# Kernel tuning notes

Hardware: AMD Instinct MI355X
Metric: run time of the kernel (lower is better)

The kernel has to match this reference:

```python
import jax, jax.numpy as jnp
import numpy as np

B, T, D = 32, 2048, 512

def setup_inputs() -> dict:
    key = jax.random.key(0)
    k1, k2, k3 = jax.random.split(key, 3)
    return {
        "query": jax.random.normal(k1, (B, D), dtype=jnp.float32),
        "key": jax.random.normal(k2, (B, T, D), dtype=jnp.float32),
        "value": jax.random.normal(k3, (B, T, D), dtype=jnp.float32),
    }

def reference(query, key, value):
    # energy: [B, T] = bmm(key [B,T,D], query [B,D,1]).squeeze
    energy = jnp.einsum("btd,bd->bt", key, query)
    attention = jax.nn.softmax(energy, axis=1)  # over T, no scaling/masking (faithful)
    # context: [B, D] = bmm(attention [B,1,T], value [B,T,D]).squeeze
    out = jnp.einsum("bt,btd->bd", attention, value)
    return (out, attention)
```

## Files before the change

kernel.cpp:

```cpp
#include <hip/hip_runtime.h>

#define B_ 32
#define T_ 2048
#define D_ 512

__global__ __launch_bounds__(256) void energy_kernel(
    const float* __restrict__ q,
    const float* __restrict__ key,
    float* __restrict__ energy)
{
    const int b    = blockIdx.x >> 6;
    const int t0   = (blockIdx.x & 63) * 32;
    const int wave = threadIdx.x >> 6;
    const int lane = threadIdx.x & 63;

    const float4 qv0 = ((const float4*)q)[b * 128 + lane];
    const float4 qv1 = ((const float4*)q)[b * 128 + 64 + lane];

    const int trow = t0 + wave * 8;
    const float4* kbase = (const float4*)key + ((size_t)b * T_ + trow) * 128;

#pragma unroll 4
    for (int r = 0; r < 8; ++r) {
        const float4 k0 = kbase[r * 128 + lane];
        const float4 k1 = kbase[r * 128 + 64 + lane];
        float acc = k0.x * qv0.x + k0.y * qv0.y + k0.z * qv0.z + k0.w * qv0.w
                  + k1.x * qv1.x + k1.y * qv1.y + k1.z * qv1.z + k1.w * qv1.w;
#pragma unroll
        for (int off = 32; off >= 1; off >>= 1)
            acc += __shfl_down(acc, off);
        if (lane == 0)
            energy[b * T_ + trow + r] = acc;
    }
}

__global__ __launch_bounds__(256) void softmax_kernel(
    const float* __restrict__ energy,
    float* __restrict__ attn)
{
    const int b = blockIdx.x;
    const int wave = threadIdx.x >> 6;
    const int lane = threadIdx.x & 63;

    const float4* e4 = (const float4*)(energy + b * T_);
    float4 v0 = e4[threadIdx.x * 2 + 0];
    float4 v1 = e4[threadIdx.x * 2 + 1];

    float m = fmaxf(fmaxf(fmaxf(v0.x, v0.y), fmaxf(v0.z, v0.w)),
                    fmaxf(fmaxf(v1.x, v1.y), fmaxf(v1.z, v1.w)));
#pragma unroll
    for (int off = 32; off >= 1; off >>= 1)
        m = fmaxf(m, __shfl_xor(m, off));
    __shared__ float redm[4];
    if (lane == 0) redm[wave] = m;
    __syncthreads();
    m = fmaxf(fmaxf(redm[0], redm[1]), fmaxf(redm[2], redm[3]));

    float4 x0, x1;
    x0.x = __expf(v0.x - m); x0.y = __expf(v0.y - m);
    x0.z = __expf(v0.z - m); x0.w = __expf(v0.w - m);
    x1.x = __expf(v1.x - m); x1.y = __expf(v1.y - m);
    x1.z = __expf(v1.z - m); x1.w = __expf(v1.w - m);
    float s = x0.x + x0.y + x0.z + x0.w + x1.x + x1.y + x1.z + x1.w;
#pragma unroll
    for (int off = 32; off >= 1; off >>= 1)
        s += __shfl_xor(s, off);
    __shared__ float reds[4];
    if (lane == 0) reds[wave] = s;
    __syncthreads();
    s = reds[0] + reds[1] + reds[2] + reds[3];

    const float inv = 1.f / s;
    x0.x *= inv; x0.y *= inv; x0.z *= inv; x0.w *= inv;
    x1.x *= inv; x1.y *= inv; x1.z *= inv; x1.w *= inv;

    float4* a4 = (float4*)(attn + b * T_);
    a4[threadIdx.x * 2 + 0] = x0;
    a4[threadIdx.x * 2 + 1] = x1;
}

__global__ __launch_bounds__(256) void context_partial_kernel(
    const float* __restrict__ attn,
    const float* __restrict__ value,
    float* __restrict__ partial)
{
    __shared__ float  attn_s[64];
    __shared__ float4 red4[128];

    const int b     = blockIdx.x >> 5;
    const int chunk = blockIdx.x & 31;
    const int t0    = chunk * 64;

    if (threadIdx.x < 64)
        attn_s[threadIdx.x] = attn[b * T_ + t0 + threadIdx.x];
    __syncthreads();

    const int tg = threadIdx.x >> 7;
    const int d4 = threadIdx.x & 127;

    const float4* v4 = (const float4*)value + ((size_t)b * T_ + t0 + tg) * 128 + d4;
    float4 acc = {0.f, 0.f, 0.f, 0.f};
#pragma unroll 8
    for (int i = 0; i < 32; ++i) {
        const float a = attn_s[2 * i + tg];
        const float4 vv = v4[i * 256];
        acc.x += a * vv.x; acc.y += a * vv.y;
        acc.z += a * vv.z; acc.w += a * vv.w;
    }

    if (tg == 1) red4[d4] = acc;
    __syncthreads();
    if (tg == 0) {
        const float4 o = red4[d4];
        acc.x += o.x; acc.y += o.y; acc.z += o.z; acc.w += o.w;
        ((float4*)partial)[((size_t)b * 32 + chunk) * 128 + d4] = acc;
    }
}

__global__ __launch_bounds__(128) void reduce_kernel(
    const float* __restrict__ partial,
    float* __restrict__ out)
{
    const int b  = blockIdx.x;
    const int d4 = threadIdx.x;
    float4 s = {0.f, 0.f, 0.f, 0.f};
#pragma unroll
    for (int c = 0; c < 32; ++c) {
        const float4 p = ((const float4*)partial)[((size_t)b * 32 + c) * 128 + d4];
        s.x += p.x; s.y += p.y; s.z += p.z; s.w += p.w;
    }
    ((float4*)out)[b * 128 + d4] = s;
}

extern "C" void kernel_launch(void* const* d_in, const int* in_sizes, int n_in,
                              void* d_out, int out_size, void* d_ws, size_t ws_size,
                              hipStream_t stream)
{
    const float* q     = (const float*)d_in[0];
    const float* key   = (const float*)d_in[1];
    const float* value = (const float*)d_in[2];

    float* out  = (float*)d_out;
    float* attn = out + B_ * D_;

    float* energy  = (float*)d_ws;
    float* partial = energy + B_ * T_;

    energy_kernel<<<B_ * 64, 256, 0, stream>>>(q, key, energy);
    softmax_kernel<<<B_, 256, 0, stream>>>(energy, attn);
    context_partial_kernel<<<B_ * 32, 256, 0, stream>>>(attn, value, partial);
    reduce_kernel<<<B_, 128, 0, stream>>>(partial, out);
}
```

Before: 288.0 us.

## Fuse four attention kernels into one cooperative kernel with grid syncs

Replaces the energy, softmax, context-partial and reduce kernels with a single cooperative kernel of 1024 blocks separated by grid-wide syncs. The aim is to remove the launch overhead and inter-kernel gaps of four launches. The costs are three grid.sync barriers, and the softmax and reduce phases run on only 32 blocks while the rest sit idle. The energy phase now does 16 rows per wave instead of 8, with half as many blocks.

```diff
diff --git a/kernel.cpp b/kernel.cpp
--- a/kernel.cpp
+++ b/kernel.cpp
@@ -1,135 +1,135 @@
 #include <hip/hip_runtime.h>
+#include <hip/hip_cooperative_groups.h>
+
+namespace cg = cooperative_groups;
 
 #define B_ 32
 #define T_ 2048
 #define D_ 512
+#define GRID_ 1024
 
-__global__ __launch_bounds__(256) void energy_kernel(
+__global__ __launch_bounds__(256, 4) void fused_attention_kernel(
     const float* __restrict__ q,
     const float* __restrict__ key,
-    float* __restrict__ energy)
-{
-    const int b    = blockIdx.x >> 6;
-    const int t0   = (blockIdx.x & 63) * 32;
-    const int wave = threadIdx.x >> 6;
-    const int lane = threadIdx.x & 63;
-
-    const float4 qv0 = ((const float4*)q)[b * 128 + lane];
-    const float4 qv1 = ((const float4*)q)[b * 128 + 64 + lane];
-
-    const int trow = t0 + wave * 8;
-    const float4* kbase = (const float4*)key + ((size_t)b * T_ + trow) * 128;
-
-#pragma unroll 4
-    for (int r = 0; r < 8; ++r) {
-        const float4 k0 = kbase[r * 128 + lane];
-        const float4 k1 = kbase[r * 128 + 64 + lane];
-        float acc = k0.x * qv0.x + k0.y * qv0.y + k0.z * qv0.z + k0.w * qv0.w
-                  + k1.x * qv1.x + k1.y * qv1.y + k1.z * qv1.z + k1.w * qv1.w;
-#pragma unroll
-        for (int off = 32; off >= 1; off >>= 1)
-            acc += __shfl_down(acc, off);
-        if (lane == 0)
-            energy[b * T_ + trow + r] = acc;
-    }
-}
-
-__global__ __launch_bounds__(256) void softmax_kernel(
-    const float* __restrict__ energy,
-    float* __restrict__ attn)
-{
-    const int b = blockIdx.x;
-    const int wave = threadIdx.x >> 6;
-    const int lane = threadIdx.x & 63;
-
-    const float4* e4 = (const float4*)(energy + b * T_);
-    float4 v0 = e4[threadIdx.x * 2 + 0];
-    float4 v1 = e4[threadIdx.x * 2 + 1];
-
-    float m = fmaxf(fmaxf(fmaxf(v0.x, v0.y), fmaxf(v0.z, v0.w)),
-                    fmaxf(fmaxf(v1.x, v1.y), fmaxf(v1.z, v1.w)));
-#pragma unroll
-    for (int off = 32; off >= 1; off >>= 1)
-        m = fmaxf(m, __shfl_xor(m, off));
-    __shared__ float redm[4];
-    if (lane == 0) redm[wave] = m;
-    __syncthreads();
-    m = fmaxf(fmaxf(redm[0], redm[1]), fmaxf(redm[2], redm[3]));
-
-    float4 x0, x1;
-    x0.x = __expf(v0.x - m); x0.y = __expf(v0.y - m);
-    x0.z = __expf(v0.z - m); x0.w = __expf(v0.w - m);
-    x1.x = __expf(v1.x - m); x1.y = __expf(v1.y - m);
-    x1.z = __expf(v1.z - m); x1.w = __expf(v1.w - m);
-    float s = x0.x + x0.y + x0.z + x0.w + x1.x + x1.y + x1.z + x1.w;
-#pragma unroll
-    for (int off = 32; off >= 1; off >>= 1)
-        s += __shfl_xor(s, off);
-    __shared__ float reds[4];
-    if (lane == 0) reds[wave] = s;
-    __syncthreads();
-    s = reds[0] + reds[1] + reds[2] + reds[3];
-
-    const float inv = 1.f / s;
-    x0.x *= inv; x0.y *= inv; x0.z *= inv; x0.w *= inv;
-    x1.x *= inv; x1.y *= inv; x1.z *= inv; x1.w *= inv;
-
-    float4* a4 = (float4*)(attn + b * T_);
-    a4[threadIdx.x * 2 + 0] = x0;
-    a4[threadIdx.x * 2 + 1] = x1;
-}
-
-__global__ __launch_bounds__(256) void context_partial_kernel(
-    const float* __restrict__ attn,
     const float* __restrict__ value,
+    float* __restrict__ out,
+    float* __restrict__ attn,
+    float* __restrict__ energy,
     float* __restrict__ partial)
 {
+    cg::grid_group grid = cg::this_grid();
+
+    __shared__ float  redm[4];
+    __shared__ float  reds[4];
     __shared__ float  attn_s[64];
     __shared__ float4 red4[128];
 
-    const int b     = blockIdx.x >> 5;
-    const int chunk = blockIdx.x & 31;
-    const int t0    = chunk * 64;
+    const int b_blk = blockIdx.x >> 5;
+    const int sub   = blockIdx.x & 31;
+    const int wave  = threadIdx.x >> 6;
+    const int lane  = threadIdx.x & 63;
 
-    if (threadIdx.x < 64)
-        attn_s[threadIdx.x] = attn[b * T_ + t0 + threadIdx.x];
-    __syncthreads();
-
-    const int tg = threadIdx.x >> 7;
-    const int d4 = threadIdx.x & 127;
-
-    const float4* v4 = (const float4*)value + ((size_t)b * T_ + t0 + tg) * 128 + d4;
-    float4 acc = {0.f, 0.f, 0.f, 0.f};
-#pragma unroll 8
-    for (int i = 0; i < 32; ++i) {
-        const float a = attn_s[2 * i + tg];
-        const float4 vv = v4[i * 256];
-        acc.x += a * vv.x; acc.y += a * vv.y;
-        acc.z += a * vv.z; acc.w += a * vv.w;
+    {
+        const float4 qv0 = ((const float4*)q)[b_blk * 128 + lane];
+        const float4 qv1 = ((const float4*)q)[b_blk * 128 + 64 + lane];
+        const int t0 = sub * 64 + wave * 16;
+        const float4* kbase = (const float4*)key + ((size_t)b_blk * T_ + t0) * 128;
+#pragma unroll 4
+        for (int r = 0; r < 16; ++r) {
+            const float4 k0 = kbase[r * 128 + lane];
+            const float4 k1 = kbase[r * 128 + 64 + lane];
+            float acc = k0.x * qv0.x + k0.y * qv0.y + k0.z * qv0.z + k0.w * qv0.w
+                      + k1.x * qv1.x + k1.y * qv1.y + k1.z * qv1.z + k1.w * qv1.w;
+#pragma unroll
+            for (int off = 32; off >= 1; off >>= 1)
+                acc += __shfl_down(acc, off);
+            if (lane == 0)
+                energy[b_blk * T_ + t0 + r] = acc;
+        }
     }
 
-    if (tg == 1) red4[d4] = acc;
-    __syncthreads();
-    if (tg == 0) {
-        const float4 o = red4[d4];
-        acc.x += o.x; acc.y += o.y; acc.z += o.z; acc.w += o.w;
-        ((float4*)partial)[((size_t)b * 32 + chunk) * 128 + d4] = acc;
+    grid.sync();
+
+    if (blockIdx.x < B_) {
+        const int b = blockIdx.x;
+        const float4* e4 = (const float4*)(energy + b * T_);
+        float4 v0 = e4[threadIdx.x * 2 + 0];
+        float4 v1 = e4[threadIdx.x * 2 + 1];
+
+        float m = fmaxf(fmaxf(fmaxf(v0.x, v0.y), fmaxf(v0.z, v0.w)),
+                        fmaxf(fmaxf(v1.x, v1.y), fmaxf(v1.z, v1.w)));
+#pragma unroll
+        for (int off = 32; off >= 1; off >>= 1)
+            m = fmaxf(m, __shfl_xor(m, off));
+        if (lane == 0) redm[wave] = m;
+        __syncthreads();
+        m = fmaxf(fmaxf(redm[0], redm[1]), fmaxf(redm[2], redm[3]));
+
+        float4 x0, x1;
+        x0.x = __expf(v0.x - m); x0.y = __expf(v0.y - m);
+        x0.z = __expf(v0.z - m); x0.w = __expf(v0.w - m);
+        x1.x = __expf(v1.x - m); x1.y = __expf(v1.y - m);
+        x1.z = __expf(v1.z - m); x1.w = __expf(v1.w - m);
+        float s = x0.x + x0.y + x0.z + x0.w + x1.x + x1.y + x1.z + x1.w;
+#pragma unroll
+        for (int off = 32; off >= 1; off >>= 1)
+            s += __shfl_xor(s, off);
+        if (lane == 0) reds[wave] = s;
+        __syncthreads();
+        s = reds[0] + reds[1] + reds[2] + reds[3];
+
+        const float inv = 1.f / s;
+        x0.x *= inv; x0.y *= inv; x0.z *= inv; x0.w *= inv;
+        x1.x *= inv; x1.y *= inv; x1.z *= inv; x1.w *= inv;
+
+        float4* a4 = (float4*)(attn + b * T_);
+        a4[threadIdx.x * 2 + 0] = x0;
+        a4[threadIdx.x * 2 + 1] = x1;
     }
-}
 
-__global__ __launch_bounds__(128) void reduce_kernel(
-    const float* __restrict__ partial,
-    float* __restrict__ out)
-{
-    const int b  = blockIdx.x;
-    const int d4 = threadIdx.x;
-    float4 s = {0.f, 0.f, 0.f, 0.f};
+    grid.sync();
+
+    {
+        const int t0 = sub * 64;
+        if (threadIdx.x < 64)
+            attn_s[threadIdx.x] = attn[b_blk * T_ + t0 + threadIdx.x];
+        __syncthreads();
+
+        const int tg = threadIdx.x >> 7;
+        const int d4 = threadIdx.x & 127;
+
+        const float4* v4 = (const float4*)value + ((size_t)b_blk * T_ + t0 + tg) * 128 + d4;
+        float4 acc = {0.f, 0.f, 0.f, 0.f};
+#pragma unroll 8
+        for (int i = 0; i < 32; ++i) {
+            const float a = attn_s[2 * i + tg];
+            const float4 vv = v4[i * 256];
+            acc.x += a * vv.x; acc.y += a * vv.y;
+            acc.z += a * vv.z; acc.w += a * vv.w;
+        }
+
+        if (tg == 1) red4[d4] = acc;
+        __syncthreads();
+        if (tg == 0) {
+            const float4 o = red4[d4];
+            acc.x += o.x; acc.y += o.y; acc.z += o.z; acc.w += o.w;
+            ((float4*)partial)[((size_t)b_blk * 32 + sub) * 128 + d4] = acc;
+        }
+    }
+
+    grid.sync();
+
+    if (blockIdx.x < B_ && threadIdx.x < 128) {
+        const int b  = blockIdx.x;
+        const int d4 = threadIdx.x;
+        float4 s = {0.f, 0.f, 0.f, 0.f};
 #pragma unroll
-    for (int c = 0; c < 32; ++c) {
-        const float4 p = ((const float4*)partial)[((size_t)b * 32 + c) * 128 + d4];
-        s.x += p.x; s.y += p.y; s.z += p.z; s.w += p.w;
+        for (int c = 0; c < 32; ++c) {
+            const float4 p = ((const float4*)partial)[((size_t)b * 32 + c) * 128 + d4];
+            s.x += p.x; s.y += p.y; s.z += p.z; s.w += p.w;
+        }
+        ((float4*)out)[b * 128 + d4] = s;
     }
-    ((float4*)out)[b * 128 + d4] = s;
 }
 
 extern "C" void kernel_launch(void* const* d_in, const int* in_sizes, int n_in,
@@ -146,8 +146,10 @@
     float* energy  = (float*)d_ws;
     float* partial = energy + B_ * T_;
 
-    energy_kernel<<<B_ * 64, 256, 0, stream>>>(q, key, energy);
-    softmax_kernel<<<B_, 256, 0, stream>>>(energy, attn);
-    context_partial_kernel<<<B_ * 32, 256, 0, stream>>>(attn, value, partial);
-    reduce_kernel<<<B_, 128, 0, stream>>>(partial, out);
+    void* args[] = {
+        (void*)&q, (void*)&key, (void*)&value,
+        (void*)&out, (void*)&attn, (void*)&energy, (void*)&partial
+    };
+    hipLaunchCooperativeKernel((void*)fused_attention_kernel,
+                               dim3(GRID_), dim3(256), args, 0, stream);
 }
```

After: 601.7 us. 109% more time.

## Fuse softmax into energy and context kernels using per-chunk online stats and atomics

Applied to the files above, without the earlier changes.

Replaces the four-kernel pipeline with two kernels. The energy kernel now also emits per-32-row max and sum-exp stats and zeroes the output. The context kernel merges those stats into a global max and sum, computes its own attention slice, and accumulates its partial context into the output with float atomics. This removes the separate softmax and reduce launches and the partial-buffer round trip, at the cost of a nondeterministic atomic summation order and some redundant stats merging in every block.

```diff
diff --git a/kernel.cpp b/kernel.cpp
--- a/kernel.cpp
+++ b/kernel.cpp
@@ -4,23 +4,32 @@
 #define T_ 2048
 #define D_ 512
 
-__global__ __launch_bounds__(256) void energy_kernel(
+__global__ __launch_bounds__(256) void energy_stats_kernel(
     const float* __restrict__ q,
     const float* __restrict__ key,
-    float* __restrict__ energy)
+    float* __restrict__ energy,
+    float* __restrict__ stats,
+    float* __restrict__ out)
 {
     const int b    = blockIdx.x >> 6;
-    const int t0   = (blockIdx.x & 63) * 32;
+    const int sub  = blockIdx.x & 63;
     const int wave = threadIdx.x >> 6;
     const int lane = threadIdx.x & 63;
+
+    if (sub == 0 && threadIdx.x < 128) {
+        const float4 z = {0.f, 0.f, 0.f, 0.f};
+        ((float4*)out)[b * 128 + threadIdx.x] = z;
+    }
+
+    __shared__ float es[32];
 
     const float4 qv0 = ((const float4*)q)[b * 128 + lane];
     const float4 qv1 = ((const float4*)q)[b * 128 + 64 + lane];
 
-    const int trow = t0 + wave * 8;
-    const float4* kbase = (const float4*)key + ((size_t)b * T_ + trow) * 128;
+    const int t0 = sub * 32 + wave * 8;
+    const float4* kbase = (const float4*)key + ((size_t)b * T_ + t0) * 128;
 
-#pragma unroll 4
+#pragma unroll
     for (int r = 0; r < 8; ++r) {
         const float4 k0 = kbase[r * 128 + lane];
         const float4 k1 = kbase[r * 128 + 64 + lane];
@@ -29,79 +38,78 @@
 #pragma unroll
         for (int off = 32; off >= 1; off >>= 1)
             acc += __shfl_down(acc, off);
-        if (lane == 0)
-            energy[b * T_ + trow + r] = acc;
+        if (lane == 0) {
+            es[wave * 8 + r] = acc;
+            energy[b * T_ + t0 + r] = acc;
+        }
+    }
+    __syncthreads();
+
+    if (threadIdx.x < 32) {
+        const float e = es[threadIdx.x];
+        float m = e;
+#pragma unroll
+        for (int off = 16; off >= 1; off >>= 1)
+            m = fmaxf(m, __shfl_xor(m, off));
+        float s = __expf(e - m);
+#pragma unroll
+        for (int off = 16; off >= 1; off >>= 1)
+            s += __shfl_xor(s, off);
+        if (threadIdx.x == 0) {
+            stats[((size_t)b * 64 + sub) * 2 + 0] = m;
+            stats[((size_t)b * 64 + sub) * 2 + 1] = s;
+        }
     }
 }
 
-__global__ __launch_bounds__(256) void softmax_kernel(
+__global__ __launch_bounds__(256) void context_kernel(
     const float* __restrict__ energy,
-    float* __restrict__ attn)
+    const float* __restrict__ stats,
+    const float* __restrict__ value,
+    float* __restrict__ attn,
+    float* __restrict__ out)
 {
-    const int b = blockIdx.x;
-    const int wave = threadIdx.x >> 6;
-    const int lane = threadIdx.x & 63;
+    const int b   = blockIdx.x >> 6;
+    const int sub = blockIdx.x & 63;
+    const int t0  = sub * 32;
+    const int tid = threadIdx.x;
 
-    const float4* e4 = (const float4*)(energy + b * T_);
-    float4 v0 = e4[threadIdx.x * 2 + 0];
-    float4 v1 = e4[threadIdx.x * 2 + 1];
-
-    float m = fmaxf(fmaxf(fmaxf(v0.x, v0.y), fmaxf(v0.z, v0.w)),
-                    fmaxf(fmaxf(v1.x, v1.y), fmaxf(v1.z, v1.w)));
-#pragma unroll
-    for (int off = 32; off >= 1; off >>= 1)
-        m = fmaxf(m, __shfl_xor(m, off));
-    __shared__ float redm[4];
-    if (lane == 0) redm[wave] = m;
-    __syncthreads();
-    m = fmaxf(fmaxf(redm[0], redm[1]), fmaxf(redm[2], redm[3]));
-
-    float4 x0, x1;
-    x0.x = __expf(v0.x - m); x0.y = __expf(v0.y - m);
-    x0.z = __expf(v0.z - m); x0.w = __expf(v0.w - m);
-    x1.x = __expf(v1.x - m); x1.y = __expf(v1.y - m);
-    x1.z = __expf(v1.z - m); x1.w = __expf(v1.w - m);
-    float s = x0.x + x0.y + x0.z + x0.w + x1.x + x1.y + x1.z + x1.w;
-#pragma unroll
-    for (int off = 32; off >= 1; off >>= 1)
-        s += __shfl_xor(s, off);
-    __shared__ float reds[4];
-    if (lane == 0) reds[wave] = s;
-    __syncthreads();
-    s = reds[0] + reds[1] + reds[2] + reds[3];
-
-    const float inv = 1.f / s;
-    x0.x *= inv; x0.y *= inv; x0.z *= inv; x0.w *= inv;
-    x1.x *= inv; x1.y *= inv; x1.z *= inv; x1.w *= inv;
-
-    float4* a4 = (float4*)(attn + b * T_);
-    a4[threadIdx.x * 2 + 0] = x0;
-    a4[threadIdx.x * 2 + 1] = x1;
-}
-
-__global__ __launch_bounds__(256) void context_partial_kernel(
-    const float* __restrict__ attn,
-    const float* __restrict__ value,
-    float* __restrict__ partial)
-{
-    __shared__ float  attn_s[64];
+    __shared__ float  MS[2];
+    __shared__ float  attn_s[32];
     __shared__ float4 red4[128];
 
-    const int b     = blockIdx.x >> 5;
-    const int chunk = blockIdx.x & 31;
-    const int t0    = chunk * 64;
+    if (tid < 64) {
+        const float m_c = stats[((size_t)b * 64 + tid) * 2 + 0];
+        const float s_c = stats[((size_t)b * 64 + tid) * 2 + 1];
+        float M = m_c;
+#pragma unroll
+        for (int off = 32; off >= 1; off >>= 1)
+            M = fmaxf(M, __shfl_xor(M, off));
+        float S = s_c * __expf(m_c - M);
+#pragma unroll
+        for (int off = 32; off >= 1; off >>= 1)
+            S += __shfl_xor(S, off);
+        if (tid == 0) { MS[0] = M; MS[1] = S; }
+    }
+    __syncthreads();
+    const float M    = MS[0];
+    const float invS = 1.f / MS[1];
 
-    if (threadIdx.x < 64)
-        attn_s[threadIdx.x] = attn[b * T_ + t0 + threadIdx.x];
+    if (tid < 32) {
+        const float e = energy[b * T_ + t0 + tid];
+        const float a = __expf(e - M) * invS;
+        attn_s[tid] = a;
+        attn[b * T_ + t0 + tid] = a;
+    }
     __syncthreads();
 
-    const int tg = threadIdx.x >> 7;
-    const int d4 = threadIdx.x & 127;
+    const int tg = tid >> 7;
+    const int d4 = tid & 127;
 
     const float4* v4 = (const float4*)value + ((size_t)b * T_ + t0 + tg) * 128 + d4;
     float4 acc = {0.f, 0.f, 0.f, 0.f};
-#pragma unroll 8
-    for (int i = 0; i < 32; ++i) {
+#pragma unroll
+    for (int i = 0; i < 16; ++i) {
         const float a = attn_s[2 * i + tg];
         const float4 vv = v4[i * 256];
         acc.x += a * vv.x; acc.y += a * vv.y;
@@ -113,23 +121,12 @@
     if (tg == 0) {
         const float4 o = red4[d4];
         acc.x += o.x; acc.y += o.y; acc.z += o.z; acc.w += o.w;
-        ((float4*)partial)[((size_t)b * 32 + chunk) * 128 + d4] = acc;
+        float* dst = out + (size_t)b * D_ + d4 * 4;
+        atomicAdd(dst + 0, acc.x);
+        atomicAdd(dst + 1, acc.y);
+        atomicAdd(dst + 2, acc.z);
+        atomicAdd(dst + 3, acc.w);
     }
-}
-
-__global__ __launch_bounds__(128) void reduce_kernel(
-    const float* __restrict__ partial,
-    float* __restrict__ out)
-{
-    const int b  = blockIdx.x;
-    const int d4 = threadIdx.x;
-    float4 s = {0.f, 0.f, 0.f, 0.f};
-#pragma unroll
-    for (int c = 0; c < 32; ++c) {
-        const float4 p = ((const float4*)partial)[((size_t)b * 32 + c) * 128 + d4];
-        s.x += p.x; s.y += p.y; s.z += p.z; s.w += p.w;
-    }
-    ((float4*)out)[b * 128 + d4] = s;
 }
 
 extern "C" void kernel_launch(void* const* d_in, const int* in_sizes, int n_in,
@@ -143,11 +140,9 @@
     float* out  = (float*)d_out;
     float* attn = out + B_ * D_;
 
-    float* energy  = (float*)d_ws;
-    float* partial = energy + B_ * T_;
+    float* energy = (float*)d_ws;
+    float* stats  = energy + B_ * T_;
 
-    energy_kernel<<<B_ * 64, 256, 0, stream>>>(q, key, energy);
-    softmax_kernel<<<B_, 256, 0, stream>>>(energy, attn);
-    context_partial_kernel<<<B_ * 32, 256, 0, stream>>>(attn, value, partial);
-    reduce_kernel<<<B_, 128, 0, stream>>>(partial, out);
+    energy_stats_kernel<<<B_ * 64, 256, 0, stream>>>(q, key, energy, stats, out);
+    context_kernel<<<B_ * 64, 256, 0, stream>>>(energy, stats, value, attn, out);
 }
```

New measurement: 284.5 us. Within noise of the previous version (-1.2%).
